# Performance work log

Hardware: AMD Instinct MI355X
Metric: run time of the kernel (lower is better)

Reference implementation:

```python
import jax, jax.numpy as jnp
import numpy as np

B, N = 4096, 128
STATE_DIM, GOAL_DIM, OBSTACLE_DIM = 6, 6, 4
VEH = 2 * STATE_DIM + GOAL_DIM  # 18


def setup_inputs() -> dict:
    key = jax.random.key(0)
    ks = jax.random.split(key, 8)
    s = lambda k, shp, fan: jax.random.normal(k, shp, jnp.float32) / np.sqrt(fan)
    return {
        "obs": jax.random.normal(ks[0], (B, 138), jnp.float32),
        "obstacles": jax.random.uniform(ks[1], (B, 5, N), jnp.float32),
        "act": jax.random.normal(ks[2], (B, 2), jnp.float32),
        "ow1": s(ks[3], (22, 256), 22),
        "ob1": jnp.zeros((256,), jnp.float32),
        "ow2": s(ks[4], (256, 256), 256),
        "ob2": jnp.zeros((256,), jnp.float32),
        "qw1": s(ks[5], (396, 256), 396),
        "qb1": jnp.zeros((256,), jnp.float32),
        "qw2": s(ks[6], (256, 256), 256),
        "qb2": jnp.zeros((256,), jnp.float32),
        "qw3": s(ks[7], (256, 1), 256),
        "qb3": jnp.zeros((1,), jnp.float32),
    }


def reference(obs, obstacles, act, ow1, ob1, ow2, ob2, qw1, qb1, qw2, qb2, qw3, qb3):
    # obs: [B, 138]; obstacles: [B, obstacle_dim+1, N]; act: [B, 2]
    veh = obs[:, :VEH]                                 # [B, 18]
    obst_data = obstacles[:, :OBSTACLE_DIM, :]         # [B, 4, N]
    mask = obstacles[:, -1, :]                         # [B, N]
    # per-obstacle features: concat broadcast vehicle state with obstacle data -> [B, N, 22]
    x = jnp.concatenate(
        [jnp.broadcast_to(veh[:, None, :], (veh.shape[0], obst_data.shape[2], VEH)),
         obst_data.transpose(0, 2, 1)], axis=-1)
    # shared obstacle MLP (ReLU on both layers, incl. output_activation)
    h = jax.nn.relu(jnp.einsum("bnf,fh->bnh", x, ow1) + ob1)
    h = jax.nn.relu(jnp.einsum("bnh,hk->bnk", h, ow2) + ob2)  # [B, N, 256]
    # masked sum-pool over obstacle axis
    pooled = jnp.einsum("bnh,bn->bh", h, mask)         # [B, 256]
    comb = jnp.concatenate([obs, pooled, act], axis=-1)  # [B, 396]
    q = jax.nn.relu(comb @ qw1 + qb1)
    q = jax.nn.relu(q @ qw2 + qb2)
    q = q @ qw3 + qb3                                   # [B, 1]
    return jnp.squeeze(q, -1)
```

## Files before the change

### kernel.cpp

```cpp
#include <hip/hip_runtime.h>
#include <hip/hip_bf16.h>


typedef __attribute__((ext_vector_type(8))) short short8;
typedef __attribute__((ext_vector_type(4))) float f32x4;

#define MFMA16(A, B, C) __builtin_amdgcn_mfma_f32_16x16x32_bf16(A, B, C, 0, 0, 0)

__device__ __forceinline__ unsigned short f2b(float f) {
  __hip_bfloat16 h = __float2bfloat16(f);
  return __builtin_bit_cast(unsigned short, h);
}

__global__ __launch_bounds__(256) void pack_weights(
    const float* __restrict__ ow1, const float* __restrict__ ow2,
    unsigned short* __restrict__ ow1q, unsigned short* __restrict__ ow2p) {
  int i = blockIdx.x * 256 + threadIdx.x;
  if (i < 8192) {
    int j = i & 7;
    int l15 = (i >> 3) & 15;
    int quad = (i >> 7) & 3;
    int mt = (i >> 9) & 15;
    int k = quad * 8 + j;
    int n_out = mt * 16 + l15;
    float v = (k < 22) ? ow1[k * 256 + n_out] : 0.f;
    ow1q[i] = f2b(v);
  }
  if (i < 65536) {
    int j = i & 7;
    int n = (i >> 3) & 255;
    int qq = i >> 11;
    int q = qq & 3;
    int kb = qq >> 2;
    int k = kb * 32 + q * 8 + j;
    ow2p[i] = f2b(ow2[k * 256 + n]);
  }
}

__global__ __launch_bounds__(256, 2) void obstacle_kernel(
    const float* __restrict__ obs, const float* __restrict__ obstacles,
    const unsigned short* __restrict__ ow1q,
    const unsigned short* __restrict__ ow2p,
    const float* __restrict__ ob1, const float* __restrict__ ob2,
    float* __restrict__ pooled_out) {
  __shared__ unsigned short xs[128 * 32];
  __shared__ unsigned short h1[128 * 256];
  __shared__ float maskL[128];
  __shared__ float b1L[256];
  __shared__ float b2L[256];
  __shared__ float vehL[24];

  const int b = blockIdx.x;
  const int tid = threadIdx.x;

  b1L[tid] = ob1[tid];
  b2L[tid] = ob2[tid];
  if (tid < 18) vehL[tid] = obs[b * 138 + tid];
  if (tid < 128) maskL[tid] = obstacles[b * 640 + 512 + tid];
  __syncthreads();

  if (tid < 128) {
    int n = tid;
    unsigned short row[32];
#pragma unroll
    for (int k = 0; k < 18; k++) row[k] = f2b(vehL[k]);
#pragma unroll
    for (int d = 0; d < 4; d++) row[18 + d] = f2b(obstacles[b * 640 + d * 128 + n]);
#pragma unroll
    for (int k = 22; k < 32; k++) row[k] = 0;
#pragma unroll
    for (int g = 0; g < 4; g++) {
      int gs = g ^ (n & 3);
#pragma unroll
      for (int j = 0; j < 8; j++) xs[n * 32 + gs * 8 + j] = row[g * 8 + j];
    }
  }
  __syncthreads();

  const int wave = tid >> 6;
  const int lane = tid & 63;
  const int quad = lane >> 4;
  const int l15 = lane & 15;

  {
    short8 wfr[4], bx[8];
#pragma unroll
    for (int i = 0; i < 4; i++) {
      int mt = wave * 4 + i;
      wfr[i] = *(const short8*)&ow1q[mt * 512 + quad * 128 + l15 * 8];
    }
#pragma unroll
    for (int nt = 0; nt < 8; nt++) {
      int n = nt * 16 + l15;
      bx[nt] = *(const short8*)&xs[n * 32 + ((quad ^ (n & 3)) << 3)];
    }
    f32x4 zero = {0.f, 0.f, 0.f, 0.f};
    f32x4 acc1[4][8];
#pragma unroll
    for (int i = 0; i < 4; i++)
#pragma unroll
      for (int nt = 0; nt < 8; nt++) acc1[i][nt] = MFMA16(wfr[i], bx[nt], zero);

#pragma unroll
    for (int i = 0; i < 4; i++) {
      int mt = wave * 4 + i;
      int nb = mt * 16 + quad * 4;
      float bias0 = b1L[nb + 0], bias1 = b1L[nb + 1];
      float bias2 = b1L[nb + 2], bias3 = b1L[nb + 3];
      int g = nb >> 3;
      int o = nb & 7;
#pragma unroll
      for (int nt = 0; nt < 8; nt++) {
        int m = nt * 16 + l15;
        float v0 = fmaxf(acc1[i][nt][0] + bias0, 0.f);
        float v1 = fmaxf(acc1[i][nt][1] + bias1, 0.f);
        float v2 = fmaxf(acc1[i][nt][2] + bias2, 0.f);
        float v3 = fmaxf(acc1[i][nt][3] + bias3, 0.f);
        uint2 pk;
        pk.x = (unsigned)f2b(v0) | ((unsigned)f2b(v1) << 16);
        pk.y = (unsigned)f2b(v2) | ((unsigned)f2b(v3) << 16);
        *(uint2*)&h1[m * 256 + (((g ^ (m & 7)) << 3) + o)] = pk;
      }
    }
  }
  __syncthreads();

  f32x4 acc[8][4];
#pragma unroll
  for (int mt = 0; mt < 8; mt++)
#pragma unroll
    for (int t = 0; t < 4; t++) acc[mt][t] = (f32x4){0.f, 0.f, 0.f, 0.f};

  const unsigned short* bp = &ow2p[(quad * 256 + wave * 64 + l15) * 8];
  short8 bcur[4], bnxt[4];
#pragma unroll
  for (int t = 0; t < 4; t++) bcur[t] = *(const short8*)&bp[t * 128];

#pragma unroll 1
  for (int kb = 0; kb < 8; kb++) {
    if (kb < 7) {
#pragma unroll
      for (int t = 0; t < 4; t++)
        bnxt[t] = *(const short8*)&bp[(kb + 1) * 8192 + t * 128];
    }
    short8 afr[8];
#pragma unroll
    for (int mt = 0; mt < 8; mt++) {
      int m = mt * 16 + l15;
      afr[mt] = *(const short8*)&h1[m * 256 + (((kb * 4 + quad) ^ (m & 7)) << 3)];
    }
#pragma unroll
    for (int mt = 0; mt < 8; mt++)
#pragma unroll
      for (int t = 0; t < 4; t++) acc[mt][t] = MFMA16(afr[mt], bcur[t], acc[mt][t]);
    if (kb < 7) {
#pragma unroll
      for (int t = 0; t < 4; t++) bcur[t] = bnxt[t];
    }
  }

#pragma unroll
  for (int t = 0; t < 4; t++) {
    int n = (wave * 4 + t) * 16 + l15;
    float bias = b2L[n];
    float s = 0.f;
#pragma unroll
    for (int mt = 0; mt < 8; mt++) {
      int mb = mt * 16 + quad * 4;
#pragma unroll
      for (int r = 0; r < 4; r++) {
        float v = fmaxf(acc[mt][t][r] + bias, 0.f);
        s += maskL[mb + r] * v;
      }
    }
    s += __shfl_xor(s, 16);
    s += __shfl_xor(s, 32);
    if (quad == 0) pooled_out[b * 256 + n] = s;
  }
}

__global__ __launch_bounds__(256) void head_mlp(
    const float* __restrict__ obs, const float* __restrict__ act,
    const float* __restrict__ pooled,
    const float* __restrict__ qw1, const float* __restrict__ qb1,
    const float* __restrict__ qw2, const float* __restrict__ qb2,
    const float* __restrict__ qw3, const float* __restrict__ qb3,
    float* __restrict__ out) {
  const int R = 4;
  __shared__ float combT[400 * R];
  __shared__ float q1T[256 * R];
  __shared__ float wred[4][R];

  const int tid = threadIdx.x;
  const int r0 = blockIdx.x * R;

#pragma unroll
  for (int r = 0; r < R; r++) {
    if (tid < 138) combT[tid * R + r] = obs[(r0 + r) * 138 + tid];
    combT[(138 + tid) * R + r] = pooled[(r0 + r) * 256 + tid];
    if (tid < 2) combT[(394 + tid) * R + r] = act[(r0 + r) * 2 + tid];
    if (tid >= 252) combT[(tid + 144) * R + r] = 0.f;
  }
  __syncthreads();

  float a[R];
  {
    float bias = qb1[tid];
#pragma unroll
    for (int r = 0; r < R; r++) a[r] = bias;
  }
  for (int k0 = 0; k0 < 392; k0 += 8) {
    float w[8];
    f32x4 c[8];
#pragma unroll
    for (int u = 0; u < 8; u++) w[u] = qw1[(k0 + u) * 256 + tid];
#pragma unroll
    for (int u = 0; u < 8; u++) c[u] = *(const f32x4*)&combT[(k0 + u) * R];
#pragma unroll
    for (int u = 0; u < 8; u++) {
      a[0] += c[u][0] * w[u]; a[1] += c[u][1] * w[u];
      a[2] += c[u][2] * w[u]; a[3] += c[u][3] * w[u];
    }
  }
#pragma unroll
  for (int u = 0; u < 4; u++) {
    int k = 392 + u;
    float w = qw1[k * 256 + tid];
    f32x4 c = *(const f32x4*)&combT[k * R];
    a[0] += c[0] * w; a[1] += c[1] * w; a[2] += c[2] * w; a[3] += c[3] * w;
  }
#pragma unroll
  for (int r = 0; r < R; r++) q1T[tid * R + r] = fmaxf(a[r], 0.f);
  __syncthreads();

  float a2[R];
  {
    float bias = qb2[tid];
#pragma unroll
    for (int r = 0; r < R; r++) a2[r] = bias;
  }
  for (int k0 = 0; k0 < 256; k0 += 8) {
    float w[8];
    f32x4 c[8];
#pragma unroll
    for (int u = 0; u < 8; u++) w[u] = qw2[(k0 + u) * 256 + tid];
#pragma unroll
    for (int u = 0; u < 8; u++) c[u] = *(const f32x4*)&q1T[(k0 + u) * R];
#pragma unroll
    for (int u = 0; u < 8; u++) {
      a2[0] += c[u][0] * w[u]; a2[1] += c[u][1] * w[u];
      a2[2] += c[u][2] * w[u]; a2[3] += c[u][3] * w[u];
    }
  }
#pragma unroll
  for (int r = 0; r < R; r++) a2[r] = fmaxf(a2[r], 0.f);

  const int wave = tid >> 6;
  const int lane = tid & 63;
  float w3 = qw3[tid];
#pragma unroll
  for (int r = 0; r < R; r++) {
    float s = a2[r] * w3;
    s += __shfl_xor(s, 1);
    s += __shfl_xor(s, 2);
    s += __shfl_xor(s, 4);
    s += __shfl_xor(s, 8);
    s += __shfl_xor(s, 16);
    s += __shfl_xor(s, 32);
    if (lane == 0) wred[wave][r] = s;
  }
  __syncthreads();
  if (tid < R)
    out[r0 + tid] = wred[0][tid] + wred[1][tid] + wred[2][tid] + wred[3][tid] + qb3[0];
}

extern "C" void kernel_launch(void* const* d_in, const int* in_sizes, int n_in,
                              void* d_out, int out_size, void* d_ws, size_t ws_size,
                              hipStream_t stream) {
  const float* obs       = (const float*)d_in[0];
  const float* obstacles = (const float*)d_in[1];
  const float* act       = (const float*)d_in[2];
  const float* ow1       = (const float*)d_in[3];
  const float* ob1       = (const float*)d_in[4];
  const float* ow2       = (const float*)d_in[5];
  const float* ob2       = (const float*)d_in[6];
  const float* qw1       = (const float*)d_in[7];
  const float* qb1       = (const float*)d_in[8];
  const float* qw2       = (const float*)d_in[9];
  const float* qb2       = (const float*)d_in[10];
  const float* qw3       = (const float*)d_in[11];
  const float* qb3       = (const float*)d_in[12];
  float* out = (float*)d_out;

  unsigned short* ow1q = (unsigned short*)d_ws;
  unsigned short* ow2p = ow1q + 8192;
  float* pooled = (float*)(ow2p + 65536);

  pack_weights<<<256, 256, 0, stream>>>(ow1, ow2, ow1q, ow2p);
  obstacle_kernel<<<4096, 256, 0, stream>>>(obs, obstacles, ow1q, ow2p, ob1, ob2,
                                            pooled);
  head_mlp<<<1024, 256, 0, stream>>>(obs, act, pooled, qw1, qb1, qw2, qb2, qw3,
                                     qb3, out);
}
```

Measured before the change: 204.6 us.

## Run head MLP on bf16 MFMA with split hi/lo precision emulation

Replaces the scalar fp32 head MLP with an MFMA kernel that processes 16 rows per block. Each fp32 operand is split into bf16 hi and lo parts, and three MFMAs per product (hi*hi, hi*lo, lo*hi) keep accuracy close to fp32. The pooled output is now written as hi/lo bf16 pairs, and the pack kernel also pre-packs qw1 and qw2 into the MFMA layout. The aim is to cut the FMA-bound head cost, at the price of three times the MFMA work, extra workspace, and a larger pack step that runs on every call.

```diff
diff --git a/kernel.cpp b/kernel.cpp
--- a/kernel.cpp
+++ b/kernel.cpp
@@ -11,10 +11,20 @@
   __hip_bfloat16 h = __float2bfloat16(f);
   return __builtin_bit_cast(unsigned short, h);
 }
+__device__ __forceinline__ float b2f(unsigned short u) {
+  unsigned v = ((unsigned)u) << 16;
+  return __builtin_bit_cast(float, v);
+}
+__device__ __forceinline__ unsigned pk2(float a, float b) {
+  return (unsigned)f2b(a) | ((unsigned)f2b(b) << 16);
+}
 
 __global__ __launch_bounds__(256) void pack_weights(
     const float* __restrict__ ow1, const float* __restrict__ ow2,
-    unsigned short* __restrict__ ow1q, unsigned short* __restrict__ ow2p) {
+    const float* __restrict__ qw1, const float* __restrict__ qw2,
+    unsigned short* __restrict__ ow1q, unsigned short* __restrict__ ow2p,
+    unsigned short* __restrict__ qw1h, unsigned short* __restrict__ qw1l,
+    unsigned short* __restrict__ qw2h, unsigned short* __restrict__ qw2l) {
   int i = blockIdx.x * 256 + threadIdx.x;
   if (i < 8192) {
     int j = i & 7;
@@ -22,18 +32,29 @@
     int quad = (i >> 7) & 3;
     int mt = (i >> 9) & 15;
     int k = quad * 8 + j;
-    int n_out = mt * 16 + l15;
-    float v = (k < 22) ? ow1[k * 256 + n_out] : 0.f;
+    float v = (k < 22) ? ow1[k * 256 + (mt * 16 + l15)] : 0.f;
     ow1q[i] = f2b(v);
   }
   if (i < 65536) {
     int j = i & 7;
     int n = (i >> 3) & 255;
     int qq = i >> 11;
-    int q = qq & 3;
-    int kb = qq >> 2;
-    int k = kb * 32 + q * 8 + j;
+    int k = (qq >> 2) * 32 + (qq & 3) * 8 + j;
     ow2p[i] = f2b(ow2[k * 256 + n]);
+    float w = qw2[k * 256 + n];
+    unsigned short h = f2b(w);
+    qw2h[i] = h;
+    qw2l[i] = f2b(w - b2f(h));
+  }
+  if (i < 106496) {
+    int j = i & 7;
+    int n = (i >> 3) & 255;
+    int qq = i >> 11;
+    int k = (qq >> 2) * 32 + (qq & 3) * 8 + j;
+    float w = (k < 396) ? qw1[k * 256 + n] : 0.f;
+    unsigned short h = f2b(w);
+    qw1h[i] = h;
+    qw1l[i] = f2b(w - b2f(h));
   }
 }
 
@@ -42,20 +63,20 @@
     const unsigned short* __restrict__ ow1q,
     const unsigned short* __restrict__ ow2p,
     const float* __restrict__ ob1, const float* __restrict__ ob2,
-    float* __restrict__ pooled_out) {
+    unsigned short* __restrict__ poolH, unsigned short* __restrict__ poolL) {
   __shared__ unsigned short xs[128 * 32];
   __shared__ unsigned short h1[128 * 256];
   __shared__ float maskL[128];
   __shared__ float b1L[256];
   __shared__ float b2L[256];
-  __shared__ float vehL[24];
+  __shared__ unsigned short vehB[32];
 
   const int b = blockIdx.x;
   const int tid = threadIdx.x;
 
   b1L[tid] = ob1[tid];
   b2L[tid] = ob2[tid];
-  if (tid < 18) vehL[tid] = obs[b * 138 + tid];
+  if (tid < 18) vehB[tid] = f2b(obs[b * 138 + tid]);
   if (tid < 128) maskL[tid] = obstacles[b * 640 + 512 + tid];
   __syncthreads();
 
@@ -63,7 +84,7 @@
     int n = tid;
     unsigned short row[32];
 #pragma unroll
-    for (int k = 0; k < 18; k++) row[k] = f2b(vehL[k]);
+    for (int k = 0; k < 18; k++) row[k] = vehB[k];
 #pragma unroll
     for (int d = 0; d < 4; d++) row[18 + d] = f2b(obstacles[b * 640 + d * 128 + n]);
 #pragma unroll
@@ -71,8 +92,7 @@
 #pragma unroll
     for (int g = 0; g < 4; g++) {
       int gs = g ^ (n & 3);
-#pragma unroll
-      for (int j = 0; j < 8; j++) xs[n * 32 + gs * 8 + j] = row[g * 8 + j];
+      *(short8*)&xs[n * 32 + gs * 8] = *(short8*)&row[g * 8];
     }
   }
   __syncthreads();
@@ -117,8 +137,8 @@
         float v2 = fmaxf(acc1[i][nt][2] + bias2, 0.f);
         float v3 = fmaxf(acc1[i][nt][3] + bias3, 0.f);
         uint2 pk;
-        pk.x = (unsigned)f2b(v0) | ((unsigned)f2b(v1) << 16);
-        pk.y = (unsigned)f2b(v2) | ((unsigned)f2b(v3) << 16);
+        pk.x = pk2(v0, v1);
+        pk.y = pk2(v2, v3);
         *(uint2*)&h1[m * 256 + (((g ^ (m & 7)) << 3) + o)] = pk;
       }
     }
@@ -175,103 +195,136 @@
     }
     s += __shfl_xor(s, 16);
     s += __shfl_xor(s, 32);
-    if (quad == 0) pooled_out[b * 256 + n] = s;
-  }
-}
-
-__global__ __launch_bounds__(256) void head_mlp(
+    if (quad == 0) {
+      unsigned short sh = f2b(s);
+      poolH[b * 256 + n] = sh;
+      poolL[b * 256 + n] = f2b(s - b2f(sh));
+    }
+  }
+}
+
+__global__ __launch_bounds__(512) void head_mfma(
     const float* __restrict__ obs, const float* __restrict__ act,
-    const float* __restrict__ pooled,
-    const float* __restrict__ qw1, const float* __restrict__ qb1,
-    const float* __restrict__ qw2, const float* __restrict__ qb2,
+    const unsigned short* __restrict__ poolH,
+    const unsigned short* __restrict__ poolL,
+    const unsigned short* __restrict__ qw1h,
+    const unsigned short* __restrict__ qw1l,
+    const unsigned short* __restrict__ qw2h,
+    const unsigned short* __restrict__ qw2l,
+    const float* __restrict__ qb1, const float* __restrict__ qb2,
     const float* __restrict__ qw3, const float* __restrict__ qb3,
     float* __restrict__ out) {
-  const int R = 4;
-  __shared__ float combT[400 * R];
-  __shared__ float q1T[256 * R];
-  __shared__ float wred[4][R];
+  const int CSTR = 424;
+  const int HSTR = 264;
+  __shared__ unsigned short combH[16 * 424], combL[16 * 424];
+  __shared__ unsigned short h1H[16 * 264], h1L[16 * 264];
+  __shared__ float wred[8][16];
 
   const int tid = threadIdx.x;
-  const int r0 = blockIdx.x * R;
-
-#pragma unroll
-  for (int r = 0; r < R; r++) {
-    if (tid < 138) combT[tid * R + r] = obs[(r0 + r) * 138 + tid];
-    combT[(138 + tid) * R + r] = pooled[(r0 + r) * 256 + tid];
-    if (tid < 2) combT[(394 + tid) * R + r] = act[(r0 + r) * 2 + tid];
-    if (tid >= 252) combT[(tid + 144) * R + r] = 0.f;
-  }
-  __syncthreads();
-
-  float a[R];
-  {
-    float bias = qb1[tid];
-#pragma unroll
-    for (int r = 0; r < R; r++) a[r] = bias;
-  }
-  for (int k0 = 0; k0 < 392; k0 += 8) {
-    float w[8];
-    f32x4 c[8];
-#pragma unroll
-    for (int u = 0; u < 8; u++) w[u] = qw1[(k0 + u) * 256 + tid];
-#pragma unroll
-    for (int u = 0; u < 8; u++) c[u] = *(const f32x4*)&combT[(k0 + u) * R];
-#pragma unroll
-    for (int u = 0; u < 8; u++) {
-      a[0] += c[u][0] * w[u]; a[1] += c[u][1] * w[u];
-      a[2] += c[u][2] * w[u]; a[3] += c[u][3] * w[u];
-    }
-  }
-#pragma unroll
-  for (int u = 0; u < 4; u++) {
-    int k = 392 + u;
-    float w = qw1[k * 256 + tid];
-    f32x4 c = *(const f32x4*)&combT[k * R];
-    a[0] += c[0] * w; a[1] += c[1] * w; a[2] += c[2] * w; a[3] += c[3] * w;
-  }
-#pragma unroll
-  for (int r = 0; r < R; r++) q1T[tid * R + r] = fmaxf(a[r], 0.f);
-  __syncthreads();
-
-  float a2[R];
-  {
-    float bias = qb2[tid];
-#pragma unroll
-    for (int r = 0; r < R; r++) a2[r] = bias;
-  }
-  for (int k0 = 0; k0 < 256; k0 += 8) {
-    float w[8];
-    f32x4 c[8];
-#pragma unroll
-    for (int u = 0; u < 8; u++) w[u] = qw2[(k0 + u) * 256 + tid];
-#pragma unroll
-    for (int u = 0; u < 8; u++) c[u] = *(const f32x4*)&q1T[(k0 + u) * R];
-#pragma unroll
-    for (int u = 0; u < 8; u++) {
-      a2[0] += c[u][0] * w[u]; a2[1] += c[u][1] * w[u];
-      a2[2] += c[u][2] * w[u]; a2[3] += c[u][3] * w[u];
-    }
-  }
-#pragma unroll
-  for (int r = 0; r < R; r++) a2[r] = fmaxf(a2[r], 0.f);
+  const int r0 = blockIdx.x * 16;
+
+  for (int idx = tid; idx < 16 * 416; idx += 512) {
+    int m = idx / 416;
+    int k = idx - m * 416;
+    unsigned short hi, lo;
+    if (k < 138) {
+      float v = obs[(r0 + m) * 138 + k];
+      hi = f2b(v);
+      lo = f2b(v - b2f(hi));
+    } else if (k < 394) {
+      hi = poolH[(r0 + m) * 256 + (k - 138)];
+      lo = poolL[(r0 + m) * 256 + (k - 138)];
+    } else if (k < 396) {
+      float v = act[(r0 + m) * 2 + (k - 394)];
+      hi = f2b(v);
+      lo = f2b(v - b2f(hi));
+    } else {
+      hi = 0; lo = 0;
+    }
+    combH[m * CSTR + k] = hi;
+    combL[m * CSTR + k] = lo;
+  }
+  __syncthreads();
 
   const int wave = tid >> 6;
   const int lane = tid & 63;
-  float w3 = qw3[tid];
-#pragma unroll
-  for (int r = 0; r < R; r++) {
-    float s = a2[r] * w3;
+  const int quad = lane >> 4;
+  const int l15 = lane & 15;
+
+  f32x4 acc[2], accm[2];
+  acc[0] = acc[1] = accm[0] = accm[1] = (f32x4){0.f, 0.f, 0.f, 0.f};
+#pragma unroll 1
+  for (int kb = 0; kb < 13; kb++) {
+    int ao = l15 * CSTR + kb * 32 + quad * 8;
+    short8 ah = *(const short8*)&combH[ao];
+    short8 al = *(const short8*)&combL[ao];
+#pragma unroll
+    for (int t = 0; t < 2; t++) {
+      int n = (wave * 2 + t) * 16 + l15;
+      int off = ((kb * 4 + quad) * 256 + n) * 8;
+      short8 bh = *(const short8*)&qw1h[off];
+      short8 bl = *(const short8*)&qw1l[off];
+      acc[t] = MFMA16(ah, bh, acc[t]);
+      accm[t] = MFMA16(ah, bl, accm[t]);
+      accm[t] = MFMA16(al, bh, accm[t]);
+    }
+  }
+#pragma unroll
+  for (int t = 0; t < 2; t++) {
+    int n = (wave * 2 + t) * 16 + l15;
+    float bias = qb1[n];
+#pragma unroll
+    for (int r = 0; r < 4; r++) {
+      int m = quad * 4 + r;
+      float v = fmaxf(acc[t][r] + accm[t][r] + bias, 0.f);
+      unsigned short hi = f2b(v);
+      h1H[m * HSTR + n] = hi;
+      h1L[m * HSTR + n] = f2b(v - b2f(hi));
+    }
+  }
+  __syncthreads();
+
+  f32x4 a2[2], a2m[2];
+  a2[0] = a2[1] = a2m[0] = a2m[1] = (f32x4){0.f, 0.f, 0.f, 0.f};
+#pragma unroll 1
+  for (int kb = 0; kb < 8; kb++) {
+    int ao = l15 * HSTR + kb * 32 + quad * 8;
+    short8 ah = *(const short8*)&h1H[ao];
+    short8 al = *(const short8*)&h1L[ao];
+#pragma unroll
+    for (int t = 0; t < 2; t++) {
+      int n = (wave * 2 + t) * 16 + l15;
+      int off = ((kb * 4 + quad) * 256 + n) * 8;
+      short8 bh = *(const short8*)&qw2h[off];
+      short8 bl = *(const short8*)&qw2l[off];
+      a2[t] = MFMA16(ah, bh, a2[t]);
+      a2m[t] = MFMA16(ah, bl, a2m[t]);
+      a2m[t] = MFMA16(al, bh, a2m[t]);
+    }
+  }
+
+#pragma unroll
+  for (int r = 0; r < 4; r++) {
+    float s = 0.f;
+#pragma unroll
+    for (int t = 0; t < 2; t++) {
+      int n = (wave * 2 + t) * 16 + l15;
+      float v = fmaxf(a2[t][r] + a2m[t][r] + qb2[n], 0.f);
+      s += v * qw3[n];
+    }
     s += __shfl_xor(s, 1);
     s += __shfl_xor(s, 2);
     s += __shfl_xor(s, 4);
     s += __shfl_xor(s, 8);
-    s += __shfl_xor(s, 16);
-    s += __shfl_xor(s, 32);
-    if (lane == 0) wred[wave][r] = s;
-  }
-  __syncthreads();
-  if (tid < R)
-    out[r0 + tid] = wred[0][tid] + wred[1][tid] + wred[2][tid] + wred[3][tid] + qb3[0];
+    if (l15 == 0) wred[wave][quad * 4 + r] = s;
+  }
+  __syncthreads();
+  if (tid < 16) {
+    float s = qb3[0];
+#pragma unroll
+    for (int w = 0; w < 8; w++) s += wred[w][tid];
+    out[r0 + tid] = s;
+  }
 }
 
 extern "C" void kernel_launch(void* const* d_in, const int* in_sizes, int n_in,
@@ -294,11 +347,17 @@
 
   unsigned short* ow1q = (unsigned short*)d_ws;
   unsigned short* ow2p = ow1q + 8192;
-  float* pooled = (float*)(ow2p + 65536);
-
-  pack_weights<<<256, 256, 0, stream>>>(ow1, ow2, ow1q, ow2p);
-  obstacle_kernel<<<4096, 256, 0, stream>>>(obs, obstacles, ow1q, ow2p, ob1, ob2,
-                                            pooled);
-  head_mlp<<<1024, 256, 0, stream>>>(obs, act, pooled, qw1, qb1, qw2, qb2, qw3,
-                                     qb3, out);
-}
+  unsigned short* qw1h = ow2p + 65536;
+  unsigned short* qw1l = qw1h + 106496;
+  unsigned short* qw2h = qw1l + 106496;
+  unsigned short* qw2l = qw2h + 65536;
+  unsigned short* poolH = qw2l + 65536;
+  unsigned short* poolL = poolH + 1048576;
+
+  pack_weights<<<416, 256, 0, stream>>>(ow1, ow2, qw1, qw2, ow1q, ow2p, qw1h,
+                                        qw1l, qw2h, qw2l);
+  obstacle_kernel<<<4096, 256, 0, stream>>>(obs, obstacles, ow1q, ow2p, ob1,
+                                            ob2, poolH, poolL);
+  head_mfma<<<256, 512, 0, stream>>>(obs, act, poolH, poolL, qw1h, qw1l, qw2h,
+                                     qw2l, qb1, qb2, qw3, qb3, out);
+}
```

Result: faster. 181.4 us (-11.3%).
